# Kernel tuning notes

Hardware: AMD Instinct MI355X
Metric: run time of the kernel (lower is better)

## Reference

```python
import jax, jax.numpy as jnp
import numpy as np

B, T = 64, 512
D_CH, D_W = 50, 300
D_IN = D_CH + D_W          # 350, GRU input dim
H = 700                    # hidden_nums
U = H // 2                 # 350, units per direction


def _gru_dir(x, mask, Wx, Wh, b, reverse):
    """Keras GRU (reset_after=True, gate order z,r,h) over time axis.
    x: [B,T,D_IN], mask: [B,T] bool, Wx: [D_IN,3U], Wh: [U,3U], b: [2,3U].
    Masked steps carry the previous state (Keras masking semantics).
    Returns hidden states [B,T,U] aligned to input time order."""
    xg = jnp.einsum('btd,dg->btg', x, Wx) + b[0]  # [B,T,3U] precomputed input gates

    def step(h, inp):
        xg_t, m = inp                      # [B,3U], [B]
        hg = h @ Wh + b[1]                 # [B,3U]
        z = jax.nn.sigmoid(xg_t[:, :U] + hg[:, :U])
        r = jax.nn.sigmoid(xg_t[:, U:2 * U] + hg[:, U:2 * U])
        hh = jnp.tanh(xg_t[:, 2 * U:] + r * hg[:, 2 * U:])
        h_new = z * h + (1.0 - z) * hh
        h = jnp.where(m[:, None], h_new, h)
        return h, h

    h0 = jnp.zeros((x.shape[0], U), x.dtype)
    _, ys = jax.lax.scan(step, h0, (xg.transpose(1, 0, 2), mask.T), reverse=reverse)
    return ys.transpose(1, 0, 2)           # [B,T,U]


def setup_inputs() -> dict:
    key = jax.random.key(0)
    ks = jax.random.split(key, 12)
    char_embedding = jax.random.normal(ks[0], (B, T, D_CH), jnp.float32)
    word_embedding = jax.random.normal(ks[1], (B, T, D_W), jnp.float32)
    sequence_length = jax.random.randint(ks[2], (B,), 1, T + 1, jnp.int32)
    mask = jnp.arange(T)[None, :] < sequence_length[:, None]  # right-padded bool mask

    def glorot(k, shape):
        lim = np.sqrt(6.0 / (shape[0] + shape[1]))
        return jax.random.uniform(k, shape, jnp.float32, -lim, lim)

    W_z = glorot(ks[3], (2, H))
    W_q = glorot(ks[4], (2, H))
    Wx_f = glorot(ks[5], (D_IN, 3 * U))
    Wh_f = glorot(ks[6], (U, 3 * U))
    b_f = jnp.zeros((2, 3 * U), jnp.float32)
    Wx_b = glorot(ks[7], (D_IN, 3 * U))
    Wh_b = glorot(ks[8], (U, 3 * U))
    b_b = jnp.zeros((2, 3 * U), jnp.float32)
    return {
        'char_embedding': char_embedding, 'word_embedding': word_embedding,
        'sequence_length': sequence_length, 'mask': mask,
        'W_z': W_z, 'W_q': W_q,
        'Wx_f': Wx_f, 'Wh_f': Wh_f, 'b_f': b_f,
        'Wx_b': Wx_b, 'Wh_b': Wh_b, 'b_b': b_b,
    }


def reference(char_embedding, word_embedding, sequence_length, mask,
              W_z, W_q, Wx_f, Wh_f, b_f, Wx_b, Wh_b, b_b):
    x = jnp.concatenate([char_embedding, word_embedding], axis=-1)   # [B,T,350]
    h_fw = _gru_dir(x, mask, Wx_f, Wh_f, b_f, reverse=False)
    h_bw = _gru_dir(x, mask, Wx_b, Wh_b, b_b, reverse=True)
    hidden_states = jnp.concatenate([h_fw, h_bw], axis=-1)           # [B,T,700]
    z_T = jax.nn.softmax(jnp.einsum('bth,ch->btc', hidden_states, W_z), axis=-1)
    z_S = jax.nn.softmax(jnp.einsum('bth,ch->btc', hidden_states, W_q), axis=-1)
    return (z_T, z_S, hidden_states)
```

## Files before the change

### kernel.cpp

```cpp
#include <hip/hip_runtime.h>
#include <hip/hip_bf16.h>
#include <math.h>

#define BB   64
#define TT   512
#define UU   350
#define GG   1050
#define DCH  50
#define DWD  300
#define DIN  350
#define CT   64
#define NCH  8

#define HBUF_OFF 0
#define HBUF_BYTES (2*2*UU*BB*4)
#define WHT_OFF  HBUF_BYTES
#define WHT_BYTES (2*GG*UU*4)
#define XG_OFF   3298560
#define XG_BYTES (2*CT*GG*BB*4)

__global__ __launch_bounds__(256) void wht_kernel(
    const float* __restrict__ Whf, const float* __restrict__ Whb,
    float* __restrict__ WhT)
{
    int idx = blockIdx.x * 256 + threadIdx.x;
    if (idx >= 2 * UU * GG) return;
    int dir = idx / (UU * GG);
    int r   = idx % (UU * GG);
    int u   = r / GG;
    int g   = r % GG;
    const float* src = dir ? Whb : Whf;
    WhT[((size_t)dir * GG + g) * UU + u] = src[u * GG + g];
}

__global__ __launch_bounds__(256) void xg_gemm_kernel(
    const float* __restrict__ ce, const float* __restrict__ we,
    const float* __restrict__ Wxf, const float* __restrict__ Wxb,
    const float* __restrict__ bf,  const float* __restrict__ bb,
    float* __restrict__ xg, int c)
{
    const int dir   = blockIdx.z;
    const int tloc  = blockIdx.y;
    const int gbase = blockIdx.x * 64;
    const int t     = dir ? (448 - c * CT + tloc) : (c * CT + tloc);
    const float* __restrict__ Wx   = dir ? Wxb : Wxf;
    const float* __restrict__ bias = dir ? bb  : bf;

    __shared__ float xs[16][68];
    __shared__ float wsh[16][68];

    const int tid = threadIdx.x;
    const int b0 = (tid & 15) * 4;
    const int g0 = (tid >> 4) * 4;
    float acc[4][4] = {};

    for (int k0 = 0; k0 < DIN; k0 += 16) {
        #pragma unroll
        for (int j = 0; j < 4; ++j) {
            int e = j * 256 + tid;
            int bbi = e >> 4, kk = e & 15;
            int k = k0 + kk;
            float v = 0.f;
            if (k < DIN)
                v = (k < DCH) ? ce[((size_t)bbi * TT + t) * DCH + k]
                              : we[((size_t)bbi * TT + t) * DWD + (k - DCH)];
            xs[kk][bbi] = v;
        }
        #pragma unroll
        for (int j = 0; j < 4; ++j) {
            int e = j * 256 + tid;
            int kk = e >> 6, gg = e & 63;
            int k = k0 + kk, g = gbase + gg;
            float v = 0.f;
            if (k < DIN && g < GG) v = Wx[(size_t)k * GG + g];
            wsh[kk][gg] = v;
        }
        __syncthreads();
        #pragma unroll
        for (int kk = 0; kk < 16; ++kk) {
            float4 xa = *(const float4*)&xs[kk][b0];
            float4 wa = *(const float4*)&wsh[kk][g0];
            acc[0][0] = fmaf(wa.x, xa.x, acc[0][0]);
            acc[0][1] = fmaf(wa.x, xa.y, acc[0][1]);
            acc[0][2] = fmaf(wa.x, xa.z, acc[0][2]);
            acc[0][3] = fmaf(wa.x, xa.w, acc[0][3]);
            acc[1][0] = fmaf(wa.y, xa.x, acc[1][0]);
            acc[1][1] = fmaf(wa.y, xa.y, acc[1][1]);
            acc[1][2] = fmaf(wa.y, xa.z, acc[1][2]);
            acc[1][3] = fmaf(wa.y, xa.w, acc[1][3]);
            acc[2][0] = fmaf(wa.z, xa.x, acc[2][0]);
            acc[2][1] = fmaf(wa.z, xa.y, acc[2][1]);
            acc[2][2] = fmaf(wa.z, xa.z, acc[2][2]);
            acc[2][3] = fmaf(wa.z, xa.w, acc[2][3]);
            acc[3][0] = fmaf(wa.w, xa.x, acc[3][0]);
            acc[3][1] = fmaf(wa.w, xa.y, acc[3][1]);
            acc[3][2] = fmaf(wa.w, xa.z, acc[3][2]);
            acc[3][3] = fmaf(wa.w, xa.w, acc[3][3]);
        }
        __syncthreads();
    }
    float* outp = xg + (size_t)((dir * CT + tloc) * GG) * BB;
    #pragma unroll
    for (int i = 0; i < 4; ++i) {
        int g = gbase + g0 + i;
        if (g < GG) {
            float bv = bias[g];
            float4 v;
            v.x = acc[i][0] + bv; v.y = acc[i][1] + bv;
            v.z = acc[i][2] + bv; v.w = acc[i][3] + bv;
            *(float4*)&outp[(size_t)g * BB + b0] = v;
        }
    }
}

__global__ __launch_bounds__(256) void gru_step_kernel(
    const float* __restrict__ xg, const float* __restrict__ WhT,
    const float* __restrict__ bf, const float* __restrict__ bb,
    const int* __restrict__ seqlen, float* __restrict__ hbuf,
    float* __restrict__ hid, int s, int c)
{
    const int b = threadIdx.x & 63;
    int up = __builtin_amdgcn_readfirstlane((int)(threadIdx.x >> 6)) + blockIdx.x * 4;
    if (up >= UU) return;
    const int dir    = blockIdx.y;
    const int slocal = s - c * CT;
    const int t      = dir ? (TT - 1 - s) : s;
    const int tloc   = dir ? (CT - 1 - slocal) : slocal;
    const float* __restrict__ bias = dir ? bb : bf;

    const float* __restrict__ hR = hbuf + (size_t)(((s & 1) * 2) + dir) * (UU * BB);
    float* __restrict__       hW = hbuf + (size_t)((((s & 1) ^ 1) * 2) + dir) * (UU * BB);

    const float* __restrict__ wz = WhT + ((size_t)dir * GG + up) * UU;
    const float* __restrict__ wr = WhT + ((size_t)dir * GG + UU + up) * UU;
    const float* __restrict__ wh = WhT + ((size_t)dir * GG + 2 * UU + up) * UU;

    float hz = bias[GG + up];
    float hr = bias[GG + UU + up];
    float hc = bias[GG + 2 * UU + up];

    #pragma unroll 10
    for (int u = 0; u < UU; ++u) {
        float hv = hR[u * BB + b];
        hz = fmaf(hv, wz[u], hz);
        hr = fmaf(hv, wr[u], hr);
        hc = fmaf(hv, wh[u], hc);
    }

    const float* xgp = xg + (size_t)((dir * CT + tloc) * GG) * BB;
    float xz = xgp[(size_t)(up)           * BB + b];
    float xr = xgp[(size_t)(up + UU)      * BB + b];
    float xh = xgp[(size_t)(up + 2 * UU)  * BB + b];

    float z   = 1.f / (1.f + expf(-(xz + hz)));
    float r   = 1.f / (1.f + expf(-(xr + hr)));
    float cnd = tanhf(xh + r * hc);
    float hprev = hR[up * BB + b];
    float hnew  = z * hprev + (1.f - z) * cnd;
    bool  m     = (t < seqlen[b]);
    hnew = m ? hnew : hprev;

    hW[up * BB + b] = hnew;
    hid[((size_t)b * TT + t) * 700 + dir * UU + up] = hnew;
}

__global__ __launch_bounds__(256) void proj_kernel(
    const float* __restrict__ Wz, const float* __restrict__ Wq,
    const float* __restrict__ hid, float* __restrict__ zT, float* __restrict__ zS)
{
    const int wave = threadIdx.x >> 6;
    const int lane = threadIdx.x & 63;
    const int row  = blockIdx.x * 4 + wave;
    const float* hp = hid + (size_t)row * 700;
    float a0 = 0.f, a1 = 0.f, a2 = 0.f, a3 = 0.f;
    #pragma unroll
    for (int i = 0; i < 11; ++i) {
        int j = i * 64 + lane;
        if (j < 700) {
            float hv = hp[j];
            a0 = fmaf(hv, Wz[j], a0);
            a1 = fmaf(hv, Wz[700 + j], a1);
            a2 = fmaf(hv, Wq[j], a2);
            a3 = fmaf(hv, Wq[700 + j], a3);
        }
    }
    #pragma unroll
    for (int off = 32; off; off >>= 1) {
        a0 += __shfl_xor(a0, off, 64);
        a1 += __shfl_xor(a1, off, 64);
        a2 += __shfl_xor(a2, off, 64);
        a3 += __shfl_xor(a3, off, 64);
    }
    if (lane == 0) {
        float m1 = fmaxf(a0, a1);
        float e0 = expf(a0 - m1), e1 = expf(a1 - m1);
        float s1 = e0 + e1;
        zT[(size_t)row * 2]     = e0 / s1;
        zT[(size_t)row * 2 + 1] = e1 / s1;
        float m2 = fmaxf(a2, a3);
        float f0 = expf(a2 - m2), f1 = expf(a3 - m2);
        float s2 = f0 + f1;
        zS[(size_t)row * 2]     = f0 / s2;
        zS[(size_t)row * 2 + 1] = f1 / s2;
    }
}

extern "C" void kernel_launch(void* const* d_in, const int* in_sizes, int n_in,
                              void* d_out, int out_size, void* d_ws, size_t ws_size,
                              hipStream_t stream)
{
    (void)in_sizes; (void)n_in; (void)out_size; (void)ws_size;
    const float* ce  = (const float*)d_in[0];
    const float* we  = (const float*)d_in[1];
    const int*   sl  = (const int*)d_in[2];
    const float* Wz  = (const float*)d_in[4];
    const float* Wq  = (const float*)d_in[5];
    const float* Wxf = (const float*)d_in[6];
    const float* Whf = (const float*)d_in[7];
    const float* bf  = (const float*)d_in[8];
    const float* Wxb = (const float*)d_in[9];
    const float* Whb = (const float*)d_in[10];
    const float* bb  = (const float*)d_in[11];

    float* out = (float*)d_out;
    float* zT  = out;
    float* zS  = out + (size_t)BB * TT * 2;
    float* hid = out + (size_t)2 * BB * TT * 2;

    char* ws = (char*)d_ws;
    float* hbuf = (float*)(ws + HBUF_OFF);
    float* WhT  = (float*)(ws + WHT_OFF);
    float* xg   = (float*)(ws + XG_OFF);

    hipMemsetAsync(hbuf, 0, HBUF_BYTES, stream);
    wht_kernel<<<dim3((2 * UU * GG + 255) / 256), 256, 0, stream>>>(Whf, Whb, WhT);

    for (int c = 0; c < NCH; ++c) {
        xg_gemm_kernel<<<dim3(17, CT, 2), 256, 0, stream>>>(ce, we, Wxf, Wxb, bf, bb, xg, c);
        for (int s = c * CT; s < (c + 1) * CT; ++s) {
            gru_step_kernel<<<dim3(88, 2), 256, 0, stream>>>(xg, WhT, bf, bb, sl, hbuf, hid, s, c);
        }
    }
    proj_kernel<<<dim3(BB * TT / 4), 256, 0, stream>>>(Wz, Wq, hid, zT, zS);
}
```

Before: 7.968 ms.

## Replace per-step GRU launches with cooperative chunk kernel using grid sync

Instead of launching one kernel per timestep (512 launches), each chunk of 64 steps runs in a single cooperative kernel of 88 blocks of 512 threads. Both directions are handled by the same block, and timesteps are separated by a threadfence plus grid.sync. This is meant to remove per-launch overhead and dispatch gaps on the sequential recurrence. The cost is the grid-wide barrier on every step and the need for all 88 blocks to be co-resident.

```diff
diff --git a/kernel.cpp b/kernel.cpp
--- a/kernel.cpp
+++ b/kernel.cpp
@@ -1,6 +1,9 @@
 #include <hip/hip_runtime.h>
 #include <hip/hip_bf16.h>
+#include <hip/hip_cooperative_groups.h>
 #include <math.h>
+
+namespace cg = cooperative_groups;
 
 #define BB   64
 #define TT   512
@@ -113,55 +116,69 @@
     }
 }
 
-__global__ __launch_bounds__(256) void gru_step_kernel(
+__global__ __launch_bounds__(512) void gru_chunk_kernel(
     const float* __restrict__ xg, const float* __restrict__ WhT,
     const float* __restrict__ bf, const float* __restrict__ bb,
     const int* __restrict__ seqlen, float* __restrict__ hbuf,
-    float* __restrict__ hid, int s, int c)
-{
-    const int b = threadIdx.x & 63;
-    int up = __builtin_amdgcn_readfirstlane((int)(threadIdx.x >> 6)) + blockIdx.x * 4;
-    if (up >= UU) return;
-    const int dir    = blockIdx.y;
-    const int slocal = s - c * CT;
-    const int t      = dir ? (TT - 1 - s) : s;
-    const int tloc   = dir ? (CT - 1 - slocal) : slocal;
+    float* __restrict__ hid, int c)
+{
+    cg::grid_group grid = cg::this_grid();
+
+    const int b   = threadIdx.x & 63;
+    const int w   = __builtin_amdgcn_readfirstlane((int)(threadIdx.x >> 6));
+    const int dir = w >> 2;
+    const int up  = blockIdx.x * 4 + (w & 3);
+    const bool act = (up < UU);
+    const int slen = seqlen[b];
+
     const float* __restrict__ bias = dir ? bb : bf;
-
-    const float* __restrict__ hR = hbuf + (size_t)(((s & 1) * 2) + dir) * (UU * BB);
-    float* __restrict__       hW = hbuf + (size_t)((((s & 1) ^ 1) * 2) + dir) * (UU * BB);
-
-    const float* __restrict__ wz = WhT + ((size_t)dir * GG + up) * UU;
-    const float* __restrict__ wr = WhT + ((size_t)dir * GG + UU + up) * UU;
-    const float* __restrict__ wh = WhT + ((size_t)dir * GG + 2 * UU + up) * UU;
-
-    float hz = bias[GG + up];
-    float hr = bias[GG + UU + up];
-    float hc = bias[GG + 2 * UU + up];
-
-    #pragma unroll 10
-    for (int u = 0; u < UU; ++u) {
-        float hv = hR[u * BB + b];
-        hz = fmaf(hv, wz[u], hz);
-        hr = fmaf(hv, wr[u], hr);
-        hc = fmaf(hv, wh[u], hc);
-    }
-
-    const float* xgp = xg + (size_t)((dir * CT + tloc) * GG) * BB;
-    float xz = xgp[(size_t)(up)           * BB + b];
-    float xr = xgp[(size_t)(up + UU)      * BB + b];
-    float xh = xgp[(size_t)(up + 2 * UU)  * BB + b];
-
-    float z   = 1.f / (1.f + expf(-(xz + hz)));
-    float r   = 1.f / (1.f + expf(-(xr + hr)));
-    float cnd = tanhf(xh + r * hc);
-    float hprev = hR[up * BB + b];
-    float hnew  = z * hprev + (1.f - z) * cnd;
-    bool  m     = (t < seqlen[b]);
-    hnew = m ? hnew : hprev;
-
-    hW[up * BB + b] = hnew;
-    hid[((size_t)b * TT + t) * 700 + dir * UU + up] = hnew;
+    const float* __restrict__ wz = WhT + ((size_t)dir * GG + (act ? up : 0)) * UU;
+    const float* __restrict__ wr = WhT + ((size_t)dir * GG + UU + (act ? up : 0)) * UU;
+    const float* __restrict__ wh = WhT + ((size_t)dir * GG + 2 * UU + (act ? up : 0)) * UU;
+    const float bz = act ? bias[GG + up] : 0.f;
+    const float br = act ? bias[GG + UU + up] : 0.f;
+    const float bh = act ? bias[GG + 2 * UU + up] : 0.f;
+
+    for (int sl = 0; sl < CT; ++sl) {
+        const int s    = c * CT + sl;
+        const int t    = dir ? (TT - 1 - s) : s;
+        const int tloc = dir ? (CT - 1 - sl) : sl;
+
+        const float* __restrict__ hR = hbuf + (size_t)(((s & 1) * 2) + dir) * (UU * BB);
+        float* __restrict__       hW = hbuf + (size_t)((((s & 1) ^ 1) * 2) + dir) * (UU * BB);
+
+        if (act) {
+            float hz = bz, hr = br, hc = bh;
+            #pragma unroll 10
+            for (int u = 0; u < UU; ++u) {
+                float hv = hR[u * BB + b];
+                hz = fmaf(hv, wz[u], hz);
+                hr = fmaf(hv, wr[u], hr);
+                hc = fmaf(hv, wh[u], hc);
+            }
+
+            const float* xgp = xg + (size_t)((dir * CT + tloc) * GG) * BB;
+            float xz = xgp[(size_t)(up)          * BB + b];
+            float xr = xgp[(size_t)(up + UU)     * BB + b];
+            float xh = xgp[(size_t)(up + 2 * UU) * BB + b];
+
+            float z   = 1.f / (1.f + expf(-(xz + hz)));
+            float r   = 1.f / (1.f + expf(-(xr + hr)));
+            float cnd = tanhf(xh + r * hc);
+            float hprev = hR[up * BB + b];
+            float hnew  = z * hprev + (1.f - z) * cnd;
+            bool  m     = (t < slen);
+            hnew = m ? hnew : hprev;
+
+            hW[up * BB + b] = hnew;
+            hid[((size_t)b * TT + t) * 700 + dir * UU + up] = hnew;
+        }
+
+        if (sl != CT - 1) {
+            __threadfence();
+            grid.sync();
+        }
+    }
 }
 
 __global__ __launch_bounds__(256) void proj_kernel(
@@ -235,11 +252,15 @@
     hipMemsetAsync(hbuf, 0, HBUF_BYTES, stream);
     wht_kernel<<<dim3((2 * UU * GG + 255) / 256), 256, 0, stream>>>(Whf, Whb, WhT);
 
+    int cvals[NCH];
     for (int c = 0; c < NCH; ++c) {
         xg_gemm_kernel<<<dim3(17, CT, 2), 256, 0, stream>>>(ce, we, Wxf, Wxb, bf, bb, xg, c);
-        for (int s = c * CT; s < (c + 1) * CT; ++s) {
-            gru_step_kernel<<<dim3(88, 2), 256, 0, stream>>>(xg, WhT, bf, bb, sl, hbuf, hid, s, c);
-        }
+        cvals[c] = c;
+        const float* xgc = xg;
+        void* args[] = { (void*)&xgc, (void*)&WhT, (void*)&bf, (void*)&bb,
+                         (void*)&sl, (void*)&hbuf, (void*)&hid, (void*)&cvals[c] };
+        hipLaunchCooperativeKernel((const void*)gru_chunk_kernel,
+                                   dim3(88), dim3(512), args, 0, stream);
     }
     proj_kernel<<<dim3(BB * TT / 4), 256, 0, stream>>>(Wz, Wq, hid, zT, zS);
 }
```

Result: slower. 23.74 ms (+197.9%).
